# Kernel tuning notes

Measured on AMD Instinct MI355X. Metric: run time of the kernel, lower is better.

## Reference

```python
import jax, jax.numpy as jnp
import numpy as np

B, S, D = 4, 1024, 768
H = 12
DK = D // H            # 64
NUM_EMB = 10
MAX_DIST = 100000.0 * 2 ** 0.5
POS_SCALE = 100000.0   # tile positions live in [0, 100000]


def setup_inputs() -> dict:
    key = jax.random.key(0)
    ks = jax.random.split(key, 12)
    query = jax.random.normal(ks[0], (B, S, D), dtype=jnp.float32)
    key_t = jax.random.normal(ks[1], (B, S, D), dtype=jnp.float32)
    value = jax.random.normal(ks[2], (B, S, D), dtype=jnp.float32)
    tile_positions = jax.random.uniform(ks[3], (B, S, 2), dtype=jnp.float32) * POS_SCALE
    # Linear weights, torch layout [out, in]; xavier_uniform init, zero bias
    lim = float(np.sqrt(6.0 / (D + D)))
    Wq = jax.random.uniform(ks[4], (D, D), minval=-lim, maxval=lim, dtype=jnp.float32)
    Wk = jax.random.uniform(ks[5], (D, D), minval=-lim, maxval=lim, dtype=jnp.float32)
    Wv = jax.random.uniform(ks[6], (D, D), minval=-lim, maxval=lim, dtype=jnp.float32)
    bq = jnp.zeros((D,), jnp.float32)
    bk = jnp.zeros((D,), jnp.float32)
    bv = jnp.zeros((D,), jnp.float32)
    emb_k = jax.random.normal(ks[7], (NUM_EMB, DK), dtype=jnp.float32)  # nn.Embedding default N(0,1)
    return {"query": query, "key": key_t, "value": value,
            "tile_positions": tile_positions,
            "Wq": Wq, "bq": bq, "Wk": Wk, "bk": bk, "Wv": Wv, "bv": bv,
            "emb_k": emb_k}


def reference(query, key, value, tile_positions, Wq, bq, Wk, bk, Wv, bv, emb_k):
    b, s, _ = query.shape
    # projections -> [B, H, S, DK]
    q = (query @ Wq.T + bq).reshape(b, s, H, DK).transpose(0, 2, 1, 3)
    k = (key   @ Wk.T + bk).reshape(b, s, H, DK).transpose(0, 2, 1, 3)
    v = (value @ Wv.T + bv).reshape(b, s, H, DK).transpose(0, 2, 1, 3)
    # pairwise distances, normalized, discretized to embedding indices
    pos = jax.lax.stop_gradient(tile_positions)
    diff = pos[:, :, None, :] - pos[:, None, :, :]          # [B,S,S,2]
    dist = jnp.sqrt(jnp.sum(diff * diff, axis=-1)) / MAX_DIST  # [B,S,S]
    idx = jnp.clip(jnp.round(dist * (NUM_EMB - 1)), 0, NUM_EMB - 1).astype(jnp.int32)
    rk = emb_k[idx]                                          # [B,S,S,DK]
    # logits: QK^T plus distance-aware key bias
    attn_logits = jnp.einsum('bhqd,bhkd->bhqk', q, k)
    attn_logits = attn_logits + jnp.einsum('bhqd,bqkd->bhqk', q, rk)
    attn_logits = attn_logits / (DK ** 0.5)
    attention = jax.nn.softmax(attn_logits, axis=-1)
    out = jnp.einsum('bhqk,bhkd->bhqd', attention, v)       # [B,H,S,DK]
    out = out.transpose(0, 2, 1, 3).reshape(b, s, -1)       # [B,S,D]
    return out
```

## Files before the change

### kernel.cpp

```cpp
#include <hip/hip_runtime.h>
#include <hip/hip_bf16.h>

#define Bsz 4
#define Ssz 1024
#define Dsz 768
#define Hn 12
#define DKsz 64
#define NUMEMB 10

#define IDX_OFF 64
#define K_OFF   4194368
#define V_OFF   10485824
#define WBF_OFF 16777280
#define XBF_OFF 20316224
#define WS_TIER_B 20316224ULL
#define WS_TIER_A 39190592ULL

#define NXz 3145728
#define NWz 589824

#define IPAD 80

typedef __attribute__((ext_vector_type(8))) short short8;
typedef __attribute__((ext_vector_type(8))) float float8;
typedef __attribute__((ext_vector_type(4))) float f32x4;
typedef __attribute__((ext_vector_type(4))) unsigned int u32x4;

__device__ __forceinline__ float bfbits2f(short u) {
    union { unsigned int i; float f; } v;
    v.i = ((unsigned int)(unsigned short)u) << 16;
    return v.f;
}
__device__ __forceinline__ unsigned short f2bf_bits(float f) {
    __hip_bfloat16 h = __float2bfloat16(f);
    return *reinterpret_cast<unsigned short*>(&h);
}

template<int CTRL>
__device__ __forceinline__ float dppf(float x) {
    int xi = __float_as_int(x);
    int r = __builtin_amdgcn_update_dpp(xi, xi, CTRL, 0xF, 0xF, true);
    return __int_as_float(r);
}
__device__ __forceinline__ float red_max16(float v) {
    v = fmaxf(v, dppf<0xB1>(v));
    v = fmaxf(v, dppf<0x4E>(v));
    v = fmaxf(v, dppf<0x124>(v));
    v = fmaxf(v, dppf<0x128>(v));
    return v;
}
__device__ __forceinline__ float red_sum16(float v) {
    v += dppf<0xB1>(v);
    v += dppf<0x4E>(v);
    v += dppf<0x124>(v);
    v += dppf<0x128>(v);
    return v;
}

template<bool BF16>
__device__ __forceinline__ float loadf(const void* base, size_t idx) {
    if constexpr (BF16) return __bfloat162float(((const __hip_bfloat16*)base)[idx]);
    else return ((const float*)base)[idx];
}
template<bool BF16>
__device__ __forceinline__ short8 load8bf(const void* base, size_t idx) {
    if constexpr (BF16) {
        return *(const short8*)((const short*)base + idx);
    } else {
        float8 f = *(const float8*)((const float*)base + idx);
        short8 r;
#pragma unroll
        for (int i = 0; i < 8; i++) r[i] = (short)f2bf_bits(f[i]);
        return r;
    }
}
template<bool BF16>
__device__ __forceinline__ float8 load8f(const void* base, size_t idx) {
    if constexpr (BF16) {
        short8 s = *(const short8*)((const short*)base + idx);
        float8 f;
#pragma unroll
        for (int i = 0; i < 8; i++) f[i] = bfbits2f(s[i]);
        return f;
    } else {
        return *(const float8*)((const float*)base + idx);
    }
}

__global__ __launch_bounds__(64) void detect_kernel(
    const unsigned int* __restrict__ q, const unsigned int* __restrict__ p,
    const unsigned int* __restrict__ w, const unsigned int* __restrict__ e,
    int* __restrict__ flags)
{
    const int which = blockIdx.x;
    const unsigned int* ptr = (which == 0) ? q : ((which == 1) ? p : ((which == 2) ? w : e));
    const int n = (which == 3) ? 320 : ((which == 1) ? 4096 : 1024);
    int cnt = 0;
    for (int i = threadIdx.x; i < n; i += 64) {
        const unsigned int ex = (ptr[i] >> 7) & 0xFF;
        cnt += (ex >= 110 && ex <= 145) ? 1 : 0;
    }
#pragma unroll
    for (int off = 1; off < 64; off <<= 1) cnt += __shfl_xor(cnt, off, 64);
    if (threadIdx.x == 0) flags[which] = (2 * cnt > n) ? 1 : 0;
}

__global__ __launch_bounds__(256) void conv_kernel(
    const void* __restrict__ X0, const void* __restrict__ X1, const void* __restrict__ X2,
    const void* __restrict__ W0, const void* __restrict__ W1, const void* __restrict__ W2,
    const int* __restrict__ flags, short* __restrict__ Xbf, short* __restrict__ Wbf,
    int doX)
{
    const long t = (long)blockIdx.x * 256 + threadIdx.x;
    const bool xb = flags[0] != 0, wb = flags[2] != 0;
    if (doX) {
        const long i8 = t * 8;
        if (i8 < (long)3 * NXz) {
            const int z = (int)(i8 / NXz);
            const long off = i8 - (long)z * NXz;
            const void* X = (z == 0) ? X0 : ((z == 1) ? X1 : X2);
            short8 v = xb ? load8bf<true>(X, off) : load8bf<false>(X, off);
            *(short8*)(Xbf + i8) = v;
        } else {
            const long j = i8 - (long)3 * NXz;
            const int z = (int)(j / NWz);
            const long off = j - (long)z * NWz;
            const void* W = (z == 0) ? W0 : ((z == 1) ? W1 : W2);
            short8 v = wb ? load8bf<true>(W, off) : load8bf<false>(W, off);
            *(short8*)(Wbf + j) = v;
        }
    } else {
        const long j = t * 8;
        const int z = (int)(j / NWz);
        const long off = j - (long)z * NWz;
        const void* W = (z == 0) ? W0 : ((z == 1) ? W1 : W2);
        short8 v = wb ? load8bf<true>(W, off) : load8bf<false>(W, off);
        *(short8*)(Wbf + j) = v;
    }
}

template<bool PB>
__device__ __forceinline__ void idx_body(
    const void* pos, unsigned char* __restrict__ idxb)
{
    const int kt = blockIdx.x, qt = blockIdx.y, b = blockIdx.z;
    const int t = threadIdx.x;
    const int r = t >> 2, cc = t & 3;
    const int q = qt * 64 + r;
    const float qx = loadf<PB>(pos, ((size_t)b * Ssz + q) * 2);
    const float qy = loadf<PB>(pos, ((size_t)b * Ssz + q) * 2 + 1);
    const float MAXD = 141421.35623730951f;
    const int k0 = kt * 64 + cc * 16;
    unsigned int w[4];
#pragma unroll
    for (int g = 0; g < 4; g++) {
        unsigned int acc = 0;
#pragma unroll
        for (int u = 0; u < 4; u++) {
            const int k = k0 + g * 4 + u;
            const float kx = loadf<PB>(pos, ((size_t)b * Ssz + k) * 2);
            const float ky = loadf<PB>(pos, ((size_t)b * Ssz + k) * 2 + 1);
            const float dx = __fsub_rn(qx, kx);
            const float dy = __fsub_rn(qy, ky);
            const float ss = __fadd_rn(__fmul_rn(dx, dx), __fmul_rn(dy, dy));
            const float dist = __fdiv_rn(sqrtf(ss), MAXD);
            const float d9 = __fmul_rn(dist, 9.0f);
            int idx = (int)rintf(d9);
            idx = idx < 0 ? 0 : (idx > NUMEMB - 1 ? NUMEMB - 1 : idx);
            acc |= ((unsigned int)idx) << (8 * u);
        }
        w[g] = acc;
    }
    u32x4 v; v[0] = w[0]; v[1] = w[1]; v[2] = w[2]; v[3] = w[3];
    *(u32x4*)(idxb + ((size_t)(b * Ssz + q)) * Ssz + k0) = v;
}

__global__ __launch_bounds__(256) void idx_kernel(
    const void* pos, const int* __restrict__ flags, unsigned char* __restrict__ idxb)
{
    if (flags[1] != 0) idx_body<true >(pos, idxb);
    else               idx_body<false>(pos, idxb);
}

template<bool XB, bool WB>
__device__ __forceinline__ void proj_body(
    const void* X, const void* W, const void* bias, bool biasbf, void* Y, bool ybf,
    int bx, int by, short* As, short* Bs)
{
    const int tid  = threadIdx.x;
    const int wave = tid >> 6;
    const int lane = tid & 63;
    const int l15  = lane & 15;
    const int quad = lane >> 4;
    const int wm = wave & 1;
    const int wn = wave >> 1;
    const int m0 = bx * 64;
    const int n0 = by * 128;

    f32x4 acc[2][4];
#pragma unroll
    for (int i = 0; i < 2; i++)
#pragma unroll
        for (int j = 0; j < 4; j++) acc[i][j] = (f32x4)0.0f;

    const int r0 = tid >> 3;
    const int cc = tid & 7;

    short8 pa0 = load8bf<XB>(X, (size_t)(m0 + r0)      * Dsz + cc * 8);
    short8 pa1 = load8bf<XB>(X, (size_t)(m0 + 32 + r0) * Dsz + cc * 8);
    short8 pb0 = load8bf<WB>(W, (size_t)(n0 + r0)      * Dsz + cc * 8);
    short8 pb1 = load8bf<WB>(W, (size_t)(n0 + 32 + r0) * Dsz + cc * 8);
    short8 pb2 = load8bf<WB>(W, (size_t)(n0 + 64 + r0) * Dsz + cc * 8);
    short8 pb3 = load8bf<WB>(W, (size_t)(n0 + 96 + r0) * Dsz + cc * 8);

    for (int kk = 0; kk < Dsz; kk += 64) {
        __syncthreads();
        *(short8*)&As[(r0)      * 72 + cc * 8] = pa0;
        *(short8*)&As[(32 + r0) * 72 + cc * 8] = pa1;
        *(short8*)&Bs[(r0)      * 72 + cc * 8] = pb0;
        *(short8*)&Bs[(32 + r0) * 72 + cc * 8] = pb1;
        *(short8*)&Bs[(64 + r0) * 72 + cc * 8] = pb2;
        *(short8*)&Bs[(96 + r0) * 72 + cc * 8] = pb3;
        __syncthreads();

        if (kk + 64 < Dsz) {
            const int k2 = kk + 64 + cc * 8;
            pa0 = load8bf<XB>(X, (size_t)(m0 + r0)      * Dsz + k2);
            pa1 = load8bf<XB>(X, (size_t)(m0 + 32 + r0) * Dsz + k2);
            pb0 = load8bf<WB>(W, (size_t)(n0 + r0)      * Dsz + k2);
            pb1 = load8bf<WB>(W, (size_t)(n0 + 32 + r0) * Dsz + k2);
            pb2 = load8bf<WB>(W, (size_t)(n0 + 64 + r0) * Dsz + k2);
            pb3 = load8bf<WB>(W, (size_t)(n0 + 96 + r0) * Dsz + k2);
        }

#pragma unroll
        for (int st = 0; st < 2; st++) {
            short8 af[2], bf[4];
#pragma unroll
            for (int i = 0; i < 2; i++)
                af[i] = *(const short8*)&As[(wm * 32 + i * 16 + l15) * 72 + st * 32 + quad * 8];
#pragma unroll
            for (int j = 0; j < 4; j++)
                bf[j] = *(const short8*)&Bs[(wn * 64 + j * 16 + l15) * 72 + st * 32 + quad * 8];
#pragma unroll
            for (int i = 0; i < 2; i++)
#pragma unroll
                for (int j = 0; j < 4; j++)
                    acc[i][j] = __builtin_amdgcn_mfma_f32_16x16x32_bf16(af[i], bf[j], acc[i][j], 0, 0, 0);
        }
    }

#pragma unroll
    for (int j = 0; j < 4; j++) {
        const int n = n0 + wn * 64 + j * 16 + l15;
        const float bv_ = biasbf ? loadf<true>(bias, n) : loadf<false>(bias, n);
#pragma unroll
        for (int i = 0; i < 2; i++) {
#pragma unroll
            for (int r = 0; r < 4; r++) {
                const int m = m0 + wm * 32 + i * 16 + quad * 4 + r;
                const float val = acc[i][j][r] + bv_;
                if (ybf) ((__hip_bfloat16*)Y)[(size_t)m * Dsz + n] = __float2bfloat16(val);
                else     ((float*)Y)[(size_t)m * Dsz + n] = val;
            }
        }
    }
}

__global__ __launch_bounds__(256) void proj_kernel(
    const void* X0, const void* X1, const void* X2,
    const void* Wq, const void* bq, const void* Wk, const void* bk,
    const void* Wv, const void* bv,
    void* Qw, void* Kw, void* Vw, const int* __restrict__ flags,
    int fx, int fw)
{
    __shared__ __align__(16) short As[64 * 72];
    __shared__ __align__(16) short Bs[128 * 72];
    const int z = blockIdx.z;
    const void* X = (z == 0) ? X0 : ((z == 1) ? X1 : X2);
    const void* W = (z == 0) ? Wq : ((z == 1) ? Wk : Wv);
    const void* B = (z == 0) ? bq : ((z == 1) ? bk : bv);
    void* Y = (z == 0) ? Qw : ((z == 1) ? Kw : Vw);
    const bool xb = fx || flags[0] != 0;
    const bool wb = fw || flags[2] != 0;
    const bool biasbf = flags[2] != 0;
    const bool ybf = (flags[0] != 0) || (z != 0);
    if (xb) { if (wb) proj_body<true , true >(X, W, B, biasbf, Y, ybf, blockIdx.x, blockIdx.y, As, Bs);
              else    proj_body<true , false>(X, W, B, biasbf, Y, ybf, blockIdx.x, blockIdx.y, As, Bs); }
    else    { if (wb) proj_body<false, true >(X, W, B, biasbf, Y, ybf, blockIdx.x, blockIdx.y, As, Bs);
              else    proj_body<false, false>(X, W, B, biasbf, Y, ybf, blockIdx.x, blockIdx.y, As, Bs); }
}

template<bool QB, bool EB>
__device__ __forceinline__ void attn_body(
    const void* Qw, const short* __restrict__ Ks, const short* __restrict__ Vs,
    const unsigned char* __restrict__ idxb, const void* __restrict__ emb, void* out,
    unsigned short* Klds, unsigned short* Vtlds, unsigned short* Plds,
    float* qe, unsigned char* Ilds)
{
    const int qt = blockIdx.x, h = blockIdx.y, b = blockIdx.z;
    const int tid  = threadIdx.x;
    const int wave = tid >> 6;
    const int lane = tid & 63;
    const int l15  = lane & 15;
    const int quad = lane >> 4;

    for (int p = tid; p < 64 * NUMEMB; p += 256) {
        const int row = p / NUMEMB, e = p - row * NUMEMB;
        const size_t qoff = ((size_t)b * Ssz + qt * 64 + row) * Dsz + h * DKsz;
        float s = 0.f;
#pragma unroll
        for (int c = 0; c < 8; c++) {
            short8 qv = load8bf<QB>(Qw, qoff + c * 8);
            float8 ef = load8f<EB>(emb, (size_t)e * DKsz + c * 8);
#pragma unroll
            for (int i = 0; i < 8; i++) s += bfbits2f(qv[i]) * ef[i];
        }
        qe[p] = s;
    }

    short8 qfrag[2];
    {
        const size_t qbase = ((size_t)b * Ssz + qt * 64 + wave * 16 + l15) * Dsz + h * DKsz;
        qfrag[0] = load8bf<QB>(Qw, qbase + quad * 8);
        qfrag[1] = load8bf<QB>(Qw, qbase + 32 + quad * 8);
    }

    float m_run[4], l_run[4];
    f32x4 oacc[4];
#pragma unroll
    for (int r = 0; r < 4; r++) { m_run[r] = -1e30f; l_run[r] = 0.f; }
#pragma unroll
    for (int j = 0; j < 4; j++) oacc[j] = (f32x4)0.0f;

    const int srow = tid >> 3, schk = tid & 7;
    const int vp   = tid >> 3;
    const int irow = tid >> 2, ichk = tid & 3;

    short8 pk0, pk1, pv0, pv1;
    u32x4 pidx;
    {
        pk0 = *(const short8*)(Ks + ((size_t)b * Ssz + srow)       * Dsz + h * DKsz + schk * 8);
        pk1 = *(const short8*)(Ks + ((size_t)b * Ssz + 32 + srow)  * Dsz + h * DKsz + schk * 8);
        pv0 = *(const short8*)(Vs + ((size_t)b * Ssz + 2 * vp)     * Dsz + h * DKsz + schk * 8);
        pv1 = *(const short8*)(Vs + ((size_t)b * Ssz + 2 * vp + 1) * Dsz + h * DKsz + schk * 8);
        pidx = *(const u32x4*)(idxb + ((size_t)(b * Ssz + irow)) * Ssz + qt * 64 + ichk * 16);
    }

    for (int it = 0; it < 16; it++) {
        __syncthreads();
        *(short8*)&Klds[(srow)      * 72 + schk * 8] = pk0;
        *(short8*)&Klds[(32 + srow) * 72 + schk * 8] = pk1;
        {
            const int ssw = (2 * vp) ^ (schk << 3);
#pragma unroll
            for (int i = 0; i < 8; i++) {
                const unsigned int dw = (unsigned int)(unsigned short)pv0[i]
                                      | ((unsigned int)(unsigned short)pv1[i] << 16);
                *(unsigned int*)&Vtlds[(schk * 8 + i) * 72 + ssw] = dw;
            }
        }
        *(u32x4*)&Ilds[irow * IPAD + ichk * 16] = pidx;
        __syncthreads();

        if (it + 1 < 16) {
            const size_t kb = ((size_t)b * Ssz + (it + 1) * 64) * Dsz + h * DKsz;
            pk0 = *(const short8*)(Ks + kb + (size_t)srow * Dsz + schk * 8);
            pk1 = *(const short8*)(Ks + kb + (size_t)(32 + srow) * Dsz + schk * 8);
            pv0 = *(const short8*)(Vs + kb + (size_t)(2 * vp) * Dsz + schk * 8);
            pv1 = *(const short8*)(Vs + kb + (size_t)(2 * vp + 1) * Dsz + schk * 8);
            pidx = *(const u32x4*)(idxb + ((size_t)(b * Ssz + (it + 1) * 64 + irow)) * Ssz + qt * 64 + ichk * 16);
        }

        f32x4 sf[4];
#pragma unroll
        for (int j = 0; j < 4; j++) sf[j] = (f32x4)0.0f;
#pragma unroll
        for (int st = 0; st < 2; st++) {
#pragma unroll
            for (int j = 0; j < 4; j++) {
                short8 kb2 = *(const short8*)&Klds[(j * 16 + l15) * 72 + st * 32 + quad * 8];
                sf[j] = __builtin_amdgcn_mfma_f32_16x16x32_bf16(qfrag[st], kb2, sf[j], 0, 0, 0);
            }
        }

        float sv[4][4];
#pragma unroll
        for (int j = 0; j < 4; j++) {
            const unsigned int iw = *(const unsigned int*)&Ilds[(j * 16 + l15) * IPAD + wave * 16 + quad * 4];
#pragma unroll
            for (int r = 0; r < 4; r++) {
                const int m = wave * 16 + quad * 4 + r;
                const int idx = (iw >> (8 * r)) & 0xFF;
                sv[r][j] = (sf[j][r] + qe[m * NUMEMB + idx]) * 0.125f;
            }
        }

        float alpha[4];
#pragma unroll
        for (int r = 0; r < 4; r++) {
            float vmax = fmaxf(fmaxf(sv[r][0], sv[r][1]), fmaxf(sv[r][2], sv[r][3]));
            vmax = red_max16(vmax);
            const float mnew = fmaxf(m_run[r], vmax);
            alpha[r] = __expf(m_run[r] - mnew);
            m_run[r] = mnew;
            float psum = 0.f;
#pragma unroll
            for (int j = 0; j < 4; j++) {
                const float p = __expf(sv[r][j] - mnew);
                sv[r][j] = p;
                psum += p;
            }
            psum = red_sum16(psum);
            l_run[r] = l_run[r] * alpha[r] + psum;
        }
#pragma unroll
        for (int j = 0; j < 4; j++) {
            f32x4 o = oacc[j];
#pragma unroll
            for (int r = 0; r < 4; r++) o[r] *= alpha[r];
            oacc[j] = o;
        }

#pragma unroll
        for (int r = 0; r < 4; r++) {
            const int m = wave * 16 + quad * 4 + r;
#pragma unroll
            for (int j = 0; j < 4; j++) {
                const int csw = (j * 16 + l15) ^ (quad << 4);
                Plds[m * 72 + csw] = f2bf_bits(sv[r][j]);
            }
        }

#pragma unroll
        for (int st = 0; st < 2; st++) {
            const int prow = wave * 16 + l15;
            const int pcsw = (st * 32 + quad * 8) ^ ((l15 >> 2) << 4);
            short8 pf = *(const short8*)&Plds[prow * 72 + pcsw];
#pragma unroll
            for (int j = 0; j < 4; j++) {
                const int d = j * 16 + l15;
                const int vsw = (st * 32 + quad * 8) ^ (((d >> 3) & 7) << 3);
                short8 vb = *(const short8*)&Vtlds[d * 72 + vsw];
                oacc[j] = __builtin_amdgcn_mfma_f32_16x16x32_bf16(pf, vb, oacc[j], 0, 0, 0);
            }
        }
    }

    __syncthreads();

#pragma unroll
    for (int r = 0; r < 4; r++) {
        const float inv = 1.0f / l_run[r];
        const int m = qt * 64 + wave * 16 + quad * 4 + r;
#pragma unroll
        for (int j = 0; j < 4; j++) {
            const int n = h * DKsz + j * 16 + l15;
            const float val = oacc[j][r] * inv;
            const size_t oidx = ((size_t)b * Ssz + m) * Dsz + n;
            if constexpr (QB) ((__hip_bfloat16*)out)[oidx] = __float2bfloat16(val);
            else              ((float*)out)[oidx] = val;
        }
    }
}

__global__ __launch_bounds__(256) void attn_kernel(
    const void* Qw, const short* __restrict__ Ks, const short* __restrict__ Vs,
    const unsigned char* __restrict__ idxb, const void* __restrict__ emb, void* out,
    const int* __restrict__ flags)
{
    __shared__ __align__(16) unsigned short Klds[64 * 72];
    __shared__ __align__(16) unsigned short Vtlds[64 * 72];
    __shared__ __align__(16) unsigned short Plds[64 * 72];
    __shared__ __align__(16) float qe[64 * NUMEMB];
    __shared__ __align__(16) unsigned char Ilds[64 * IPAD];

    const bool qb = flags[0] != 0, eb = flags[3] != 0;
    if (qb) { if (eb) attn_body<true , true >(Qw, Ks, Vs, idxb, emb, out, Klds, Vtlds, Plds, qe, Ilds);
              else    attn_body<true , false>(Qw, Ks, Vs, idxb, emb, out, Klds, Vtlds, Plds, qe, Ilds); }
    else    { if (eb) attn_body<false, true >(Qw, Ks, Vs, idxb, emb, out, Klds, Vtlds, Plds, qe, Ilds);
              else    attn_body<false, false>(Qw, Ks, Vs, idxb, emb, out, Klds, Vtlds, Plds, qe, Ilds); }
}

extern "C" void kernel_launch(void* const* d_in, const int* in_sizes, int n_in,
                              void* d_out, int out_size, void* d_ws, size_t ws_size,
                              hipStream_t stream) {
    const void* query = d_in[0];
    const void* key   = d_in[1];
    const void* value = d_in[2];
    const void* tpos  = d_in[3];
    const void* Wq    = d_in[4];
    const void* bq    = d_in[5];
    const void* Wk    = d_in[6];
    const void* bk    = d_in[7];
    const void* Wv    = d_in[8];
    const void* bv    = d_in[9];
    const void* emb   = d_in[10];

    int*           flags = (int*)d_ws;
    unsigned char* idxb  = (unsigned char*)d_ws + IDX_OFF;
    void*          Kw    = (char*)d_ws + K_OFF;
    void*          Vw    = (char*)d_ws + V_OFF;
    short*         Wbf   = (short*)((char*)d_ws + WBF_OFF);
    short*         Xbf   = (short*)((char*)d_ws + XBF_OFF);
    void*          Qw    = d_out;

    const bool tierA = ws_size >= WS_TIER_A;
    const bool tierB = !tierA && ws_size >= WS_TIER_B;

    detect_kernel<<<4, 64, 0, stream>>>(
        (const unsigned int*)query, (const unsigned int*)tpos,
        (const unsigned int*)Wq, (const unsigned int*)emb, flags);

    if (tierA)
        conv_kernel<<<5472, 256, 0, stream>>>(query, key, value, Wq, Wk, Wv, flags, Xbf, Wbf, 1);
    else if (tierB)
        conv_kernel<<<864, 256, 0, stream>>>(query, key, value, Wq, Wk, Wv, flags, Xbf, Wbf, 0);

    idx_kernel<<<dim3(16, 16, Bsz), 256, 0, stream>>>(tpos, flags, idxb);

    if (tierA)
        proj_kernel<<<dim3(64, 6, 3), 256, 0, stream>>>(
            Xbf, Xbf + NXz, Xbf + 2 * NXz,
            Wbf, bq, Wbf + NWz, bk, Wbf + 2 * NWz, bv,
            Qw, Kw, Vw, flags, 1, 1);
    else if (tierB)
        proj_kernel<<<dim3(64, 6, 3), 256, 0, stream>>>(
            query, key, value,
            Wbf, bq, Wbf + NWz, bk, Wbf + 2 * NWz, bv,
            Qw, Kw, Vw, flags, 0, 1);
    else
        proj_kernel<<<dim3(64, 6, 3), 256, 0, stream>>>(
            query, key, value, Wq, bq, Wk, bk, Wv, bv,
            Qw, Kw, Vw, flags, 0, 0);

    attn_kernel<<<dim3(16, Hn, Bsz), 256, 0, stream>>>(
        Qw, (const short*)Kw, (const short*)Vw, idxb, emb, d_out, flags);
}
```

Before: 221.0 us.

## Split attention over key halves with combine kernel; stage positions in LDS

The attention kernel now splits the key range into two halves per (batch, head, q-tile) when the large workspace tier is available. This doubles the grid from 768 to 1536 blocks to improve occupancy across CUs. Each half writes its running max, sum and unnormalized bf16 output to workspace, and a new combine kernel merges them with log-sum-exp weights. The idx kernel also stages q/k positions in shared memory instead of reloading them per element, and the qe bias is pre-scaled so the logit becomes a single fma. The cost is an extra launch, extra workspace traffic, and bf16 rounding of the partial outputs.

```diff
diff --git a/kernel.cpp b/kernel.cpp
--- a/kernel.cpp
+++ b/kernel.cpp
@@ -15,6 +15,8 @@
 #define XBF_OFF 20316224
 #define WS_TIER_B 20316224ULL
 #define WS_TIER_A 39190592ULL
+#define PML_OFF 16777280
+#define PO_OFF  17563712
 
 #define NXz 3145728
 #define NWz 589824
@@ -141,14 +143,23 @@
 
 template<bool PB>
 __device__ __forceinline__ void idx_body(
-    const void* pos, unsigned char* __restrict__ idxb)
+    const void* pos, unsigned char* __restrict__ idxb, float* qp, float* kp)
 {
     const int kt = blockIdx.x, qt = blockIdx.y, b = blockIdx.z;
     const int t = threadIdx.x;
+    if (t < 128) {
+        const int row = t >> 1, c = t & 1;
+        qp[t] = loadf<PB>(pos, ((size_t)b * Ssz + qt * 64 + row) * 2 + c);
+    } else {
+        const int t2 = t - 128;
+        const int row = t2 >> 1, c = t2 & 1;
+        kp[t2] = loadf<PB>(pos, ((size_t)b * Ssz + kt * 64 + row) * 2 + c);
+    }
+    __syncthreads();
+
     const int r = t >> 2, cc = t & 3;
     const int q = qt * 64 + r;
-    const float qx = loadf<PB>(pos, ((size_t)b * Ssz + q) * 2);
-    const float qy = loadf<PB>(pos, ((size_t)b * Ssz + q) * 2 + 1);
+    const float qx = qp[r * 2], qy = qp[r * 2 + 1];
     const float MAXD = 141421.35623730951f;
     const int k0 = kt * 64 + cc * 16;
     unsigned int w[4];
@@ -157,9 +168,8 @@
         unsigned int acc = 0;
 #pragma unroll
         for (int u = 0; u < 4; u++) {
-            const int k = k0 + g * 4 + u;
-            const float kx = loadf<PB>(pos, ((size_t)b * Ssz + k) * 2);
-            const float ky = loadf<PB>(pos, ((size_t)b * Ssz + k) * 2 + 1);
+            const int kl = cc * 16 + g * 4 + u;
+            const float kx = kp[kl * 2], ky = kp[kl * 2 + 1];
             const float dx = __fsub_rn(qx, kx);
             const float dy = __fsub_rn(qy, ky);
             const float ss = __fadd_rn(__fmul_rn(dx, dx), __fmul_rn(dy, dy));
@@ -178,8 +188,10 @@
 __global__ __launch_bounds__(256) void idx_kernel(
     const void* pos, const int* __restrict__ flags, unsigned char* __restrict__ idxb)
 {
-    if (flags[1] != 0) idx_body<true >(pos, idxb);
-    else               idx_body<false>(pos, idxb);
+    __shared__ __align__(16) float qp[128];
+    __shared__ __align__(16) float kp[128];
+    if (flags[1] != 0) idx_body<true >(pos, idxb, qp, kp);
+    else               idx_body<false>(pos, idxb, qp, kp);
 }
 
 template<bool XB, bool WB>
@@ -291,14 +303,19 @@
               else    proj_body<false, false>(X, W, B, biasbf, Y, ybf, blockIdx.x, blockIdx.y, As, Bs); }
 }
 
-template<bool QB, bool EB>
+template<bool QB, bool EB, bool SPLIT>
 __device__ __forceinline__ void attn_body(
     const void* Qw, const short* __restrict__ Ks, const short* __restrict__ Vs,
     const unsigned char* __restrict__ idxb, const void* __restrict__ emb, void* out,
+    float* __restrict__ pml, unsigned short* __restrict__ pO,
     unsigned short* Klds, unsigned short* Vtlds, unsigned short* Plds,
     float* qe, unsigned char* Ilds)
 {
-    const int qt = blockIdx.x, h = blockIdx.y, b = blockIdx.z;
+    const int qt = blockIdx.x, h = blockIdx.y;
+    const int b    = SPLIT ? (blockIdx.z >> 1) : blockIdx.z;
+    const int half = SPLIT ? (blockIdx.z & 1) : 0;
+    const int itBeg = SPLIT ? half * 8 : 0;
+    const int itEnd = itBeg + (SPLIT ? 8 : 16);
     const int tid  = threadIdx.x;
     const int wave = tid >> 6;
     const int lane = tid & 63;
@@ -316,7 +333,7 @@
 #pragma unroll
             for (int i = 0; i < 8; i++) s += bfbits2f(qv[i]) * ef[i];
         }
-        qe[p] = s;
+        qe[p] = s * 0.125f;
     }
 
     short8 qfrag[2];
@@ -340,14 +357,15 @@
     short8 pk0, pk1, pv0, pv1;
     u32x4 pidx;
     {
-        pk0 = *(const short8*)(Ks + ((size_t)b * Ssz + srow)       * Dsz + h * DKsz + schk * 8);
-        pk1 = *(const short8*)(Ks + ((size_t)b * Ssz + 32 + srow)  * Dsz + h * DKsz + schk * 8);
-        pv0 = *(const short8*)(Vs + ((size_t)b * Ssz + 2 * vp)     * Dsz + h * DKsz + schk * 8);
-        pv1 = *(const short8*)(Vs + ((size_t)b * Ssz + 2 * vp + 1) * Dsz + h * DKsz + schk * 8);
-        pidx = *(const u32x4*)(idxb + ((size_t)(b * Ssz + irow)) * Ssz + qt * 64 + ichk * 16);
-    }
-
-    for (int it = 0; it < 16; it++) {
+        const size_t kb = ((size_t)b * Ssz + itBeg * 64) * Dsz + h * DKsz;
+        pk0 = *(const short8*)(Ks + kb + (size_t)srow * Dsz + schk * 8);
+        pk1 = *(const short8*)(Ks + kb + (size_t)(32 + srow) * Dsz + schk * 8);
+        pv0 = *(const short8*)(Vs + kb + (size_t)(2 * vp) * Dsz + schk * 8);
+        pv1 = *(const short8*)(Vs + kb + (size_t)(2 * vp + 1) * Dsz + schk * 8);
+        pidx = *(const u32x4*)(idxb + ((size_t)(b * Ssz + itBeg * 64 + irow)) * Ssz + qt * 64 + ichk * 16);
+    }
+
+    for (int it = itBeg; it < itEnd; it++) {
         __syncthreads();
         *(short8*)&Klds[(srow)      * 72 + schk * 8] = pk0;
         *(short8*)&Klds[(32 + srow) * 72 + schk * 8] = pk1;
@@ -363,7 +381,7 @@
         *(u32x4*)&Ilds[irow * IPAD + ichk * 16] = pidx;
         __syncthreads();
 
-        if (it + 1 < 16) {
+        if (it + 1 < itEnd) {
             const size_t kb = ((size_t)b * Ssz + (it + 1) * 64) * Dsz + h * DKsz;
             pk0 = *(const short8*)(Ks + kb + (size_t)srow * Dsz + schk * 8);
             pk1 = *(const short8*)(Ks + kb + (size_t)(32 + srow) * Dsz + schk * 8);
@@ -392,7 +410,7 @@
             for (int r = 0; r < 4; r++) {
                 const int m = wave * 16 + quad * 4 + r;
                 const int idx = (iw >> (8 * r)) & 0xFF;
-                sv[r][j] = (sf[j][r] + qe[m * NUMEMB + idx]) * 0.125f;
+                sv[r][j] = fmaf(sf[j][r], 0.125f, qe[m * NUMEMB + idx]);
             }
         }
 
@@ -447,27 +465,57 @@
         }
     }
 
-    __syncthreads();
-
-#pragma unroll
-    for (int r = 0; r < 4; r++) {
-        const float inv = 1.0f / l_run[r];
-        const int m = qt * 64 + wave * 16 + quad * 4 + r;
-#pragma unroll
-        for (int j = 0; j < 4; j++) {
-            const int n = h * DKsz + j * 16 + l15;
-            const float val = oacc[j][r] * inv;
-            const size_t oidx = ((size_t)b * Ssz + m) * Dsz + n;
-            if constexpr (QB) ((__hip_bfloat16*)out)[oidx] = __float2bfloat16(val);
-            else              ((float*)out)[oidx] = val;
-        }
-    }
+    if constexpr (SPLIT) {
+        const size_t rbase = (((size_t)(b * 2 + half) * Hn + h) * Ssz + qt * 64);
+#pragma unroll
+        for (int r = 0; r < 4; r++) {
+            const int m = wave * 16 + quad * 4 + r;
+            if (l15 == 0) {
+                pml[(rbase + m) * 2]     = m_run[r];
+                pml[(rbase + m) * 2 + 1] = l_run[r];
+            }
+#pragma unroll
+            for (int j = 0; j < 4; j++)
+                pO[(rbase + m) * DKsz + j * 16 + l15] = f2bf_bits(oacc[j][r]);
+        }
+    } else {
+        __syncthreads();
+#pragma unroll
+        for (int r = 0; r < 4; r++) {
+            const float inv = 1.0f / l_run[r];
+            const int m = qt * 64 + wave * 16 + quad * 4 + r;
+#pragma unroll
+            for (int j = 0; j < 4; j++) {
+                const int n = h * DKsz + j * 16 + l15;
+                const float val = oacc[j][r] * inv;
+                const size_t oidx = ((size_t)b * Ssz + m) * Dsz + n;
+                if constexpr (QB) ((__hip_bfloat16*)out)[oidx] = __float2bfloat16(val);
+                else              ((float*)out)[oidx] = val;
+            }
+        }
+    }
+}
+
+template<bool SPLIT>
+__device__ __forceinline__ void attn_dispatch(
+    const void* Qw, const short* Ks, const short* Vs,
+    const unsigned char* idxb, const void* emb, void* out,
+    float* pml, unsigned short* pO, const int* flags,
+    unsigned short* Klds, unsigned short* Vtlds, unsigned short* Plds,
+    float* qe, unsigned char* Ilds)
+{
+    const bool qb = flags[0] != 0, eb = flags[3] != 0;
+    if (qb) { if (eb) attn_body<true , true , SPLIT>(Qw, Ks, Vs, idxb, emb, out, pml, pO, Klds, Vtlds, Plds, qe, Ilds);
+              else    attn_body<true , false, SPLIT>(Qw, Ks, Vs, idxb, emb, out, pml, pO, Klds, Vtlds, Plds, qe, Ilds); }
+    else    { if (eb) attn_body<false, true , SPLIT>(Qw, Ks, Vs, idxb, emb, out, pml, pO, Klds, Vtlds, Plds, qe, Ilds);
+              else    attn_body<false, false, SPLIT>(Qw, Ks, Vs, idxb, emb, out, pml, pO, Klds, Vtlds, Plds, qe, Ilds); }
 }
 
 __global__ __launch_bounds__(256) void attn_kernel(
     const void* Qw, const short* __restrict__ Ks, const short* __restrict__ Vs,
     const unsigned char* __restrict__ idxb, const void* __restrict__ emb, void* out,
-    const int* __restrict__ flags)
+    float* __restrict__ pml, unsigned short* __restrict__ pO,
+    const int* __restrict__ flags, int split)
 {
     __shared__ __align__(16) unsigned short Klds[64 * 72];
     __shared__ __align__(16) unsigned short Vtlds[64 * 72];
@@ -475,11 +523,45 @@
     __shared__ __align__(16) float qe[64 * NUMEMB];
     __shared__ __align__(16) unsigned char Ilds[64 * IPAD];
 
-    const bool qb = flags[0] != 0, eb = flags[3] != 0;
-    if (qb) { if (eb) attn_body<true , true >(Qw, Ks, Vs, idxb, emb, out, Klds, Vtlds, Plds, qe, Ilds);
-              else    attn_body<true , false>(Qw, Ks, Vs, idxb, emb, out, Klds, Vtlds, Plds, qe, Ilds); }
-    else    { if (eb) attn_body<false, true >(Qw, Ks, Vs, idxb, emb, out, Klds, Vtlds, Plds, qe, Ilds);
-              else    attn_body<false, false>(Qw, Ks, Vs, idxb, emb, out, Klds, Vtlds, Plds, qe, Ilds); }
+    if (split) attn_dispatch<true >(Qw, Ks, Vs, idxb, emb, out, pml, pO, flags, Klds, Vtlds, Plds, qe, Ilds);
+    else       attn_dispatch<false>(Qw, Ks, Vs, idxb, emb, out, pml, pO, flags, Klds, Vtlds, Plds, qe, Ilds);
+}
+
+__global__ __launch_bounds__(256) void combine_kernel(
+    const float* __restrict__ pml, const unsigned short* __restrict__ pO,
+    void* out, const int* __restrict__ flags)
+{
+    const int qt = blockIdx.x, h = blockIdx.y, b = blockIdx.z;
+    const int t = threadIdx.x;
+    const int q = t >> 2, dg = t & 3;
+    const int qg = qt * 64 + q;
+    const size_t r1 = (((size_t)(b * 2 + 0) * Hn + h) * Ssz + qg);
+    const size_t r2 = (((size_t)(b * 2 + 1) * Hn + h) * Ssz + qg);
+    const float m1 = pml[r1 * 2], l1 = pml[r1 * 2 + 1];
+    const float m2 = pml[r2 * 2], l2 = pml[r2 * 2 + 1];
+    const float mm = fmaxf(m1, m2);
+    const float w1 = __expf(m1 - mm), w2 = __expf(m2 - mm);
+    const float inv = 1.0f / (w1 * l1 + w2 * l2);
+    const bool obf = flags[0] != 0;
+#pragma unroll
+    for (int c = 0; c < 2; c++) {
+        short8 o1 = *(const short8*)(pO + r1 * DKsz + dg * 16 + c * 8);
+        short8 o2 = *(const short8*)(pO + r2 * DKsz + dg * 16 + c * 8);
+        const size_t obase = ((size_t)b * Ssz + qg) * Dsz + h * DKsz + dg * 16 + c * 8;
+        if (obf) {
+#pragma unroll
+            for (int i = 0; i < 8; i++) {
+                const float v = (w1 * bfbits2f(o1[i]) + w2 * bfbits2f(o2[i])) * inv;
+                ((__hip_bfloat16*)out)[obase + i] = __float2bfloat16(v);
+            }
+        } else {
+            float8 v;
+#pragma unroll
+            for (int i = 0; i < 8; i++)
+                v[i] = (w1 * bfbits2f(o1[i]) + w2 * bfbits2f(o2[i])) * inv;
+            *(float8*)((float*)out + obase) = v;
+        }
+    }
 }
 
 extern "C" void kernel_launch(void* const* d_in, const int* in_sizes, int n_in,
@@ -497,13 +579,15 @@
     const void* bv    = d_in[9];
     const void* emb   = d_in[10];
 
-    int*           flags = (int*)d_ws;
-    unsigned char* idxb  = (unsigned char*)d_ws + IDX_OFF;
-    void*          Kw    = (char*)d_ws + K_OFF;
-    void*          Vw    = (char*)d_ws + V_OFF;
-    short*         Wbf   = (short*)((char*)d_ws + WBF_OFF);
-    short*         Xbf   = (short*)((char*)d_ws + XBF_OFF);
-    void*          Qw    = d_out;
+    int*            flags = (int*)d_ws;
+    unsigned char*  idxb  = (unsigned char*)d_ws + IDX_OFF;
+    void*           Kw    = (char*)d_ws + K_OFF;
+    void*           Vw    = (char*)d_ws + V_OFF;
+    short*          Wbf   = (short*)((char*)d_ws + WBF_OFF);
+    short*          Xbf   = (short*)((char*)d_ws + XBF_OFF);
+    float*          pml   = (float*)((char*)d_ws + PML_OFF);
+    unsigned short* pO    = (unsigned short*)((char*)d_ws + PO_OFF);
+    void*           Qw    = d_out;
 
     const bool tierA = ws_size >= WS_TIER_A;
     const bool tierB = !tierA && ws_size >= WS_TIER_B;
@@ -534,6 +618,12 @@
             query, key, value, Wq, bq, Wk, bk, Wv, bv,
             Qw, Kw, Vw, flags, 0, 0);
 
-    attn_kernel<<<dim3(16, Hn, Bsz), 256, 0, stream>>>(
-        Qw, (const short*)Kw, (const short*)Vw, idxb, emb, d_out, flags);
-}
+    if (tierA) {
+        attn_kernel<<<dim3(16, Hn, Bsz * 2), 256, 0, stream>>>(
+            Qw, (const short*)Kw, (const short*)Vw, idxb, emb, d_out, pml, pO, flags, 1);
+        combine_kernel<<<dim3(16, Hn, Bsz), 256, 0, stream>>>(pml, pO, d_out, flags);
+    } else {
+        attn_kernel<<<dim3(16, Hn, Bsz), 256, 0, stream>>>(
+            Qw, (const short*)Kw, (const short*)Vw, idxb, emb, d_out, pml, pO, flags, 0);
+    }
+}
```

Result: slower. 232.5 us (+5.2%).

## Double-buffer attention tiles with direct global-to-LDS loads and pre-transposed V

Applied to the files above, without the earlier changes.

Adds a separate kernel that writes V transposed per head into workspace. A new attention kernel then streams K, V^T and distance-index tiles into double-buffered, XOR-swizzled LDS using global_load_lds, so the next tile loads while the current one is computed. The positional bias is pre-scaled so the logit becomes a single fma, and idx_kernel now stages positions in shared memory. The cost is an extra launch and an extra global round trip for V, and the new path runs only when the large workspace tier is available.

```diff
diff --git a/kernel.cpp b/kernel.cpp
--- a/kernel.cpp
+++ b/kernel.cpp
@@ -13,6 +13,7 @@
 #define V_OFF   10485824
 #define WBF_OFF 16777280
 #define XBF_OFF 20316224
+#define VT_OFF  20316224
 #define WS_TIER_B 20316224ULL
 #define WS_TIER_A 39190592ULL
 
@@ -34,6 +35,12 @@
 __device__ __forceinline__ unsigned short f2bf_bits(float f) {
     __hip_bfloat16 h = __float2bfloat16(f);
     return *reinterpret_cast<unsigned short*>(&h);
+}
+
+__device__ __forceinline__ void dma16(const void* g, void* l) {
+    __builtin_amdgcn_global_load_lds(
+        (const __attribute__((address_space(1))) unsigned int*)g,
+        (__attribute__((address_space(3))) unsigned int*)l, 16, 0, 0);
 }
 
 template<int CTRL>
@@ -141,14 +148,23 @@
 
 template<bool PB>
 __device__ __forceinline__ void idx_body(
-    const void* pos, unsigned char* __restrict__ idxb)
+    const void* pos, unsigned char* __restrict__ idxb, float* qp, float* kp)
 {
     const int kt = blockIdx.x, qt = blockIdx.y, b = blockIdx.z;
     const int t = threadIdx.x;
+    if (t < 128) {
+        const int row = t >> 1, c = t & 1;
+        qp[t] = loadf<PB>(pos, ((size_t)b * Ssz + qt * 64 + row) * 2 + c);
+    } else {
+        const int t2 = t - 128;
+        const int row = t2 >> 1, c = t2 & 1;
+        kp[t2] = loadf<PB>(pos, ((size_t)b * Ssz + kt * 64 + row) * 2 + c);
+    }
+    __syncthreads();
+
     const int r = t >> 2, cc = t & 3;
     const int q = qt * 64 + r;
-    const float qx = loadf<PB>(pos, ((size_t)b * Ssz + q) * 2);
-    const float qy = loadf<PB>(pos, ((size_t)b * Ssz + q) * 2 + 1);
+    const float qx = qp[r * 2], qy = qp[r * 2 + 1];
     const float MAXD = 141421.35623730951f;
     const int k0 = kt * 64 + cc * 16;
     unsigned int w[4];
@@ -157,9 +173,8 @@
         unsigned int acc = 0;
 #pragma unroll
         for (int u = 0; u < 4; u++) {
-            const int k = k0 + g * 4 + u;
-            const float kx = loadf<PB>(pos, ((size_t)b * Ssz + k) * 2);
-            const float ky = loadf<PB>(pos, ((size_t)b * Ssz + k) * 2 + 1);
+            const int kl = cc * 16 + g * 4 + u;
+            const float kx = kp[kl * 2], ky = kp[kl * 2 + 1];
             const float dx = __fsub_rn(qx, kx);
             const float dy = __fsub_rn(qy, ky);
             const float ss = __fadd_rn(__fmul_rn(dx, dx), __fmul_rn(dy, dy));
@@ -178,8 +193,10 @@
 __global__ __launch_bounds__(256) void idx_kernel(
     const void* pos, const int* __restrict__ flags, unsigned char* __restrict__ idxb)
 {
-    if (flags[1] != 0) idx_body<true >(pos, idxb);
-    else               idx_body<false>(pos, idxb);
+    __shared__ __align__(16) float qp[128];
+    __shared__ __align__(16) float kp[128];
+    if (flags[1] != 0) idx_body<true >(pos, idxb, qp, kp);
+    else               idx_body<false>(pos, idxb, qp, kp);
 }
 
 template<bool XB, bool WB>
@@ -291,12 +308,37 @@
               else    proj_body<false, false>(X, W, B, biasbf, Y, ybf, blockIdx.x, blockIdx.y, As, Bs); }
 }
 
+__global__ __launch_bounds__(256) void vt_kernel(
+    const short* __restrict__ Vw, short* __restrict__ Vtg)
+{
+    __shared__ __align__(16) unsigned short t[64 * 72];
+    const int stile = blockIdx.x, h = blockIdx.y, b = blockIdx.z;
+    const int tid = threadIdx.x;
+    const int vp = tid >> 3, chunk = tid & 7;
+    const size_t base = ((size_t)b * Ssz + stile * 64) * Dsz + h * DKsz;
+    short8 pv0 = *(const short8*)(Vw + base + (size_t)(2 * vp)     * Dsz + chunk * 8);
+    short8 pv1 = *(const short8*)(Vw + base + (size_t)(2 * vp + 1) * Dsz + chunk * 8);
+#pragma unroll
+    for (int i = 0; i < 8; i++) {
+        const unsigned int dw = (unsigned int)(unsigned short)pv0[i]
+                              | ((unsigned int)(unsigned short)pv1[i] << 16);
+        *(unsigned int*)&t[(chunk * 8 + i) * 72 + 2 * vp] = dw;
+    }
+    __syncthreads();
+    const int drow = tid >> 2, c2 = tid & 3;
+#pragma unroll
+    for (int cc = 0; cc < 2; cc++) {
+        const int c = c2 + cc * 4;
+        short8 o = *(const short8*)&t[drow * 72 + c * 8];
+        *(short8*)(Vtg + (((size_t)(b * Hn + h) * 64 + drow) * Ssz) + stile * 64 + c * 8) = o;
+    }
+}
+
 template<bool QB, bool EB>
-__device__ __forceinline__ void attn_body(
-    const void* Qw, const short* __restrict__ Ks, const short* __restrict__ Vs,
+__device__ __forceinline__ void attn_dma_body(
+    const void* Qw, const short* __restrict__ Ks, const short* __restrict__ Vtg,
     const unsigned char* __restrict__ idxb, const void* __restrict__ emb, void* out,
-    unsigned short* Klds, unsigned short* Vtlds, unsigned short* Plds,
-    float* qe, unsigned char* Ilds)
+    short* Kl, short* Vtl, unsigned char* Il, unsigned short* Pl, float* qe)
 {
     const int qt = blockIdx.x, h = blockIdx.y, b = blockIdx.z;
     const int tid  = threadIdx.x;
@@ -305,6 +347,11 @@
     const int l15  = lane & 15;
     const int quad = lane >> 4;
 
+    const int cK = (lane & 7) ^ ((lane >> 3) & 7);
+    const int cI = (lane & 3) ^ ((lane >> 2) & 3);
+    const int krow = lane >> 3;
+    const int irow = lane >> 2;
+
     for (int p = tid; p < 64 * NUMEMB; p += 256) {
         const int row = p / NUMEMB, e = p - row * NUMEMB;
         const size_t qoff = ((size_t)b * Ssz + qt * 64 + row) * Dsz + h * DKsz;
@@ -316,7 +363,188 @@
 #pragma unroll
             for (int i = 0; i < 8; i++) s += bfbits2f(qv[i]) * ef[i];
         }
-        qe[p] = s;
+        qe[p] = s * 0.125f;
+    }
+
+    short8 qfrag[2];
+    {
+        const size_t qbase = ((size_t)b * Ssz + qt * 64 + wave * 16 + l15) * Dsz + h * DKsz;
+        qfrag[0] = load8bf<QB>(Qw, qbase + quad * 8);
+        qfrag[1] = load8bf<QB>(Qw, qbase + 32 + quad * 8);
+    }
+
+    float m_run[4], l_run[4];
+    f32x4 oacc[4];
+#pragma unroll
+    for (int r = 0; r < 4; r++) { m_run[r] = -1e30f; l_run[r] = 0.f; }
+#pragma unroll
+    for (int j = 0; j < 4; j++) oacc[j] = (f32x4)0.0f;
+
+    auto issue = [&](int it, int buf) {
+        short* kb = Kl + buf * 4096;
+        short* vb = Vtl + buf * 4096;
+        unsigned char* ib = Il + buf * 4096;
+#pragma unroll
+        for (int hh = 0; hh < 2; hh++) {
+            const size_t gk = ((size_t)(b * Ssz + it * 64 + hh * 32 + wave * 8 + krow)) * Dsz + h * DKsz + cK * 8;
+            dma16(Ks + gk, (char*)kb + hh * 4096 + wave * 1024);
+            const size_t gv = (((size_t)(b * Hn + h) * 64) + hh * 32 + wave * 8 + krow) * Ssz + it * 64 + cK * 8;
+            dma16(Vtg + gv, (char*)vb + hh * 4096 + wave * 1024);
+        }
+        const size_t gi = ((size_t)(b * Ssz + it * 64 + wave * 16 + irow)) * Ssz + qt * 64 + cI * 16;
+        dma16(idxb + gi, (char*)ib + wave * 1024);
+    };
+
+    issue(0, 0);
+
+    for (int it = 0; it < 16; it++) {
+        const int cur = it & 1;
+        __syncthreads();
+        if (it + 1 < 16) issue(it + 1, cur ^ 1);
+
+        const short* kb = Kl + cur * 4096;
+        const short* vb = Vtl + cur * 4096;
+        const unsigned char* ib = Il + cur * 4096;
+
+        f32x4 sf[4];
+#pragma unroll
+        for (int j = 0; j < 4; j++) sf[j] = (f32x4)0.0f;
+#pragma unroll
+        for (int st = 0; st < 2; st++) {
+#pragma unroll
+            for (int j = 0; j < 4; j++) {
+                const int pc = (st * 4 + quad) ^ (l15 & 7);
+                short8 kf = *(const short8*)(kb + (j * 16 + l15) * 64 + pc * 8);
+                sf[j] = __builtin_amdgcn_mfma_f32_16x16x32_bf16(qfrag[st], kf, sf[j], 0, 0, 0);
+            }
+        }
+
+        float sv[4][4];
+#pragma unroll
+        for (int j = 0; j < 4; j++) {
+            const int row = j * 16 + l15;
+            const int pd = ((wave ^ (row & 3)) << 2) | quad;
+            const unsigned int iw = *(const unsigned int*)(ib + row * 64 + pd * 4);
+#pragma unroll
+            for (int r = 0; r < 4; r++) {
+                const int m = wave * 16 + quad * 4 + r;
+                const int idx = (iw >> (8 * r)) & 0xFF;
+                sv[r][j] = fmaf(sf[j][r], 0.125f, qe[m * NUMEMB + idx]);
+            }
+        }
+
+        float alpha[4];
+#pragma unroll
+        for (int r = 0; r < 4; r++) {
+            float vmax = fmaxf(fmaxf(sv[r][0], sv[r][1]), fmaxf(sv[r][2], sv[r][3]));
+            vmax = red_max16(vmax);
+            const float mnew = fmaxf(m_run[r], vmax);
+            alpha[r] = __expf(m_run[r] - mnew);
+            m_run[r] = mnew;
+            float psum = 0.f;
+#pragma unroll
+            for (int j = 0; j < 4; j++) {
+                const float p = __expf(sv[r][j] - mnew);
+                sv[r][j] = p;
+                psum += p;
+            }
+            psum = red_sum16(psum);
+            l_run[r] = l_run[r] * alpha[r] + psum;
+        }
+#pragma unroll
+        for (int j = 0; j < 4; j++) {
+            f32x4 o = oacc[j];
+#pragma unroll
+            for (int r = 0; r < 4; r++) o[r] *= alpha[r];
+            oacc[j] = o;
+        }
+
+#pragma unroll
+        for (int r = 0; r < 4; r++) {
+            const int m = wave * 16 + quad * 4 + r;
+#pragma unroll
+            for (int j = 0; j < 4; j++) {
+                const int csw = (j * 16 + l15) ^ (quad << 4);
+                Pl[m * 72 + csw] = f2bf_bits(sv[r][j]);
+            }
+        }
+
+#pragma unroll
+        for (int st = 0; st < 2; st++) {
+            const int prow = wave * 16 + l15;
+            const int pcsw = (st * 32 + quad * 8) ^ ((l15 >> 2) << 4);
+            short8 pf = *(const short8*)&Pl[prow * 72 + pcsw];
+#pragma unroll
+            for (int j = 0; j < 4; j++) {
+                const int d = j * 16 + l15;
+                const int pc = (st * 4 + quad) ^ (d & 7);
+                short8 vf = *(const short8*)(vb + d * 64 + pc * 8);
+                oacc[j] = __builtin_amdgcn_mfma_f32_16x16x32_bf16(pf, vf, oacc[j], 0, 0, 0);
+            }
+        }
+    }
+
+    __syncthreads();
+
+#pragma unroll
+    for (int r = 0; r < 4; r++) {
+        const float inv = 1.0f / l_run[r];
+        const int m = qt * 64 + wave * 16 + quad * 4 + r;
+#pragma unroll
+        for (int j = 0; j < 4; j++) {
+            const int n = h * DKsz + j * 16 + l15;
+            const float val = oacc[j][r] * inv;
+            const size_t oidx = ((size_t)b * Ssz + m) * Dsz + n;
+            if constexpr (QB) ((__hip_bfloat16*)out)[oidx] = __float2bfloat16(val);
+            else              ((float*)out)[oidx] = val;
+        }
+    }
+}
+
+__global__ __launch_bounds__(256) void attn_dma_kernel(
+    const void* Qw, const short* __restrict__ Ks, const short* __restrict__ Vtg,
+    const unsigned char* __restrict__ idxb, const void* __restrict__ emb, void* out,
+    const int* __restrict__ flags)
+{
+    __shared__ __align__(16) short Kl[2 * 4096];
+    __shared__ __align__(16) short Vtl[2 * 4096];
+    __shared__ __align__(16) unsigned char Il[2 * 4096];
+    __shared__ __align__(16) unsigned short Pl[64 * 72];
+    __shared__ __align__(16) float qe[64 * NUMEMB];
+
+    const bool qb = flags[0] != 0, eb = flags[3] != 0;
+    if (qb) { if (eb) attn_dma_body<true , true >(Qw, Ks, Vtg, idxb, emb, out, Kl, Vtl, Il, Pl, qe);
+              else    attn_dma_body<true , false>(Qw, Ks, Vtg, idxb, emb, out, Kl, Vtl, Il, Pl, qe); }
+    else    { if (eb) attn_dma_body<false, true >(Qw, Ks, Vtg, idxb, emb, out, Kl, Vtl, Il, Pl, qe);
+              else    attn_dma_body<false, false>(Qw, Ks, Vtg, idxb, emb, out, Kl, Vtl, Il, Pl, qe); }
+}
+
+template<bool QB, bool EB>
+__device__ __forceinline__ void attn_reg_body(
+    const void* Qw, const short* __restrict__ Ks, const short* __restrict__ Vs,
+    const unsigned char* __restrict__ idxb, const void* __restrict__ emb, void* out,
+    unsigned short* Klds, unsigned short* Vtlds, unsigned short* Plds,
+    float* qe, unsigned char* Ilds)
+{
+    const int qt = blockIdx.x, h = blockIdx.y, b = blockIdx.z;
+    const int tid  = threadIdx.x;
+    const int wave = tid >> 6;
+    const int lane = tid & 63;
+    const int l15  = lane & 15;
+    const int quad = lane >> 4;
+
+    for (int p = tid; p < 64 * NUMEMB; p += 256) {
+        const int row = p / NUMEMB, e = p - row * NUMEMB;
+        const size_t qoff = ((size_t)b * Ssz + qt * 64 + row) * Dsz + h * DKsz;
+        float s = 0.f;
+#pragma unroll
+        for (int c = 0; c < 8; c++) {
+            short8 qv = load8bf<QB>(Qw, qoff + c * 8);
+            float8 ef = load8f<EB>(emb, (size_t)e * DKsz + c * 8);
+#pragma unroll
+            for (int i = 0; i < 8; i++) s += bfbits2f(qv[i]) * ef[i];
+        }
+        qe[p] = s * 0.125f;
     }
 
     short8 qfrag[2];
@@ -392,7 +620,7 @@
             for (int r = 0; r < 4; r++) {
                 const int m = wave * 16 + quad * 4 + r;
                 const int idx = (iw >> (8 * r)) & 0xFF;
-                sv[r][j] = (sf[j][r] + qe[m * NUMEMB + idx]) * 0.125f;
+                sv[r][j] = fmaf(sf[j][r], 0.125f, qe[m * NUMEMB + idx]);
             }
         }
 
@@ -441,8 +669,8 @@
             for (int j = 0; j < 4; j++) {
                 const int d = j * 16 + l15;
                 const int vsw = (st * 32 + quad * 8) ^ (((d >> 3) & 7) << 3);
-                short8 vb = *(const short8*)&Vtlds[d * 72 + vsw];
-                oacc[j] = __builtin_amdgcn_mfma_f32_16x16x32_bf16(pf, vb, oacc[j], 0, 0, 0);
+                short8 vbf = *(const short8*)&Vtlds[d * 72 + vsw];
+                oacc[j] = __builtin_amdgcn_mfma_f32_16x16x32_bf16(pf, vbf, oacc[j], 0, 0, 0);
             }
         }
     }
@@ -464,7 +692,7 @@
     }
 }
 
-__global__ __launch_bounds__(256) void attn_kernel(
+__global__ __launch_bounds__(256) void attn_reg_kernel(
     const void* Qw, const short* __restrict__ Ks, const short* __restrict__ Vs,
     const unsigned char* __restrict__ idxb, const void* __restrict__ emb, void* out,
     const int* __restrict__ flags)
@@ -476,10 +704,10 @@
     __shared__ __align__(16) unsigned char Ilds[64 * IPAD];
 
     const bool qb = flags[0] != 0, eb = flags[3] != 0;
-    if (qb) { if (eb) attn_body<true , true >(Qw, Ks, Vs, idxb, emb, out, Klds, Vtlds, Plds, qe, Ilds);
-              else    attn_body<true , false>(Qw, Ks, Vs, idxb, emb, out, Klds, Vtlds, Plds, qe, Ilds); }
-    else    { if (eb) attn_body<false, true >(Qw, Ks, Vs, idxb, emb, out, Klds, Vtlds, Plds, qe, Ilds);
-              else    attn_body<false, false>(Qw, Ks, Vs, idxb, emb, out, Klds, Vtlds, Plds, qe, Ilds); }
+    if (qb) { if (eb) attn_reg_body<true , true >(Qw, Ks, Vs, idxb, emb, out, Klds, Vtlds, Plds, qe, Ilds);
+              else    attn_reg_body<true , false>(Qw, Ks, Vs, idxb, emb, out, Klds, Vtlds, Plds, qe, Ilds); }
+    else    { if (eb) attn_reg_body<false, true >(Qw, Ks, Vs, idxb, emb, out, Klds, Vtlds, Plds, qe, Ilds);
+              else    attn_reg_body<false, false>(Qw, Ks, Vs, idxb, emb, out, Klds, Vtlds, Plds, qe, Ilds); }
 }
 
 extern "C" void kernel_launch(void* const* d_in, const int* in_sizes, int n_in,
@@ -503,6 +731,7 @@
     void*          Vw    = (char*)d_ws + V_OFF;
     short*         Wbf   = (short*)((char*)d_ws + WBF_OFF);
     short*         Xbf   = (short*)((char*)d_ws + XBF_OFF);
+    short*         Vtg   = (short*)((char*)d_ws + VT_OFF);
     void*          Qw    = d_out;
 
     const bool tierA = ws_size >= WS_TIER_A;
@@ -534,6 +763,12 @@
             query, key, value, Wq, bq, Wk, bk, Wv, bv,
             Qw, Kw, Vw, flags, 0, 0);
 
-    attn_kernel<<<dim3(16, Hn, Bsz), 256, 0, stream>>>(
-        Qw, (const short*)Kw, (const short*)Vw, idxb, emb, d_out, flags);
-}
+    if (tierA) {
+        vt_kernel<<<dim3(16, Hn, Bsz), 256, 0, stream>>>((const short*)Vw, Vtg);
+        attn_dma_kernel<<<dim3(16, Hn, Bsz), 256, 0, stream>>>(
+            Qw, (const short*)Kw, (const short*)Vtg, idxb, emb, d_out, flags);
+    } else {
+        attn_reg_kernel<<<dim3(16, Hn, Bsz), 256, 0, stream>>>(
+            Qw, (const short*)Kw, (const short*)Vw, idxb, emb, d_out, flags);
+    }
+}
```

New measurement: 230.6 us. 1.04x slower.
